# Kernel tuning notes

Measured on AMD Instinct MI355X. Metric: run time of the kernel, lower is better.

The kernel has to match this reference:

```python
import jax, jax.numpy as jnp
import numpy as np

N = 100000   # nodes
E = 300000   # edges
D_IN = 128   # input feature dim
H = 256      # hidden dim
L = 4        # GIN layers
G = 512      # graphs in batch
BN_EPS = 1e-5


def setup_inputs() -> dict:
    key = jax.random.key(0)
    ks = jax.random.split(key, 12)
    s = 0.02
    return {
        "x": jax.random.normal(ks[0], (N, D_IN), jnp.float32),
        "edge_index": jax.random.randint(ks[1], (2, E), 0, N, dtype=jnp.int32),
        "batch": jnp.sort(jax.random.randint(ks[2], (N,), 0, G, dtype=jnp.int32)),
        "W_in": jax.random.normal(ks[3], (D_IN, H), jnp.float32) * s,
        "b_in": jnp.zeros((H,), jnp.float32),
        "eps": jnp.zeros((L,), jnp.float32),           # GINConv train_eps init = 0
        "W1": jax.random.normal(ks[4], (L, H, 2 * H), jnp.float32) * s,
        "b1": jnp.zeros((L, 2 * H), jnp.float32),
        "W2": jax.random.normal(ks[5], (L, 2 * H, H), jnp.float32) * s,
        "b2": jnp.zeros((L, H), jnp.float32),
        "gamma": jnp.ones((L, H), jnp.float32),
        "beta": jnp.zeros((L, H), jnp.float32),
        "Wp1": jax.random.normal(ks[6], (H, H // 2), jnp.float32) * s,
        "bp1": jnp.zeros((H // 2,), jnp.float32),
        "Wp2": jax.random.normal(ks[7], (H // 2, 1), jnp.float32) * s,
        "bp2": jnp.zeros((1,), jnp.float32),
    }


def reference(x, edge_index, batch, W_in, b_in, eps, W1, b1, W2, b2,
              gamma, beta, Wp1, bp1, Wp2, bp2):
    src, dst = edge_index[0], edge_index[1]

    # input projection + relu
    h = jax.nn.relu(x @ W_in + b_in)  # [N, H]

    def layer(h, p):
        e, w1, bb1, w2, bb2, g, bt = p
        # GINConv: sum-aggregate neighbor messages at destination nodes
        agg = jax.ops.segment_sum(h[src], dst, num_segments=N)  # [N, H]
        z = (1.0 + e) * h + agg
        # GIN MLP: H -> 2H -> H
        z = jax.nn.relu(z @ w1 + bb1) @ w2 + bb2
        # BatchNorm over node dim (training-mode batch statistics, biased var)
        mu = jnp.mean(z, axis=0)
        var = jnp.var(z, axis=0)
        z = g * (z - mu) * jax.lax.rsqrt(var + BN_EPS) + bt
        return jax.nn.relu(z), None

    h, _ = jax.lax.scan(layer, h, (eps, W1, b1, W2, b2, gamma, beta))

    # global mean pool per graph
    sums = jax.ops.segment_sum(h, batch, num_segments=G)                       # [G, H]
    counts = jax.ops.segment_sum(jnp.ones((N, 1), h.dtype), batch, num_segments=G)
    pooled = sums / jnp.maximum(counts, 1.0)

    # predictor head (dropout is identity in eval)
    out = jax.nn.relu(pooled @ Wp1 + bp1) @ Wp2 + bp2  # [G, 1]
    return out
```

## Files before the change

kernel.cpp:

```cpp
#include <hip/hip_runtime.h>

#define NN 100000
#define NP 100096
#define EE 300000
#define DIN 128
#define HD  256
#define HD2 512
#define NL  4
#define NG  512
#define BN_EPS 1e-5f

typedef __attribute__((ext_vector_type(8))) short s8v;
typedef __attribute__((ext_vector_type(4))) float f4v;

typedef unsigned short ushort_t;

static __device__ inline ushort_t f2bf(float f) {
    unsigned u = __float_as_uint(f);
    unsigned r = (u + 0x7fffu + ((u >> 16) & 1u)) >> 16;
    return (ushort_t)r;
}
static __device__ inline float bf2f(ushort_t h) {
    return __uint_as_float(((unsigned)h) << 16);
}
static __device__ inline float blo(unsigned v) { return __uint_as_float(v << 16); }
static __device__ inline float bhi(unsigned v) { return __uint_as_float(v & 0xffff0000u); }

#define GLOAD_LDS16(g, l) __builtin_amdgcn_global_load_lds( \
    (const __attribute__((address_space(1))) unsigned int*)(const void*)(g), \
    (__attribute__((address_space(3))) unsigned int*)(void*)(l), 16, 0, 0)

#define WAITCNT_VM8 0xF78
#define WAITCNT_VM4 0xF74
#define WAITCNT_VM0 0xF70

__global__ __launch_bounds__(256) void gemm_bf16(
    const ushort_t* __restrict__ A, int lda,
    const ushort_t* __restrict__ BT, int ldb,
    const float* __restrict__ bias,
    ushort_t* __restrict__ C, int ldc,
    int K, int doRelu,
    int doStats, float* __restrict__ stats, int Mvalid)
{
    extern __shared__ char smem[];
    ushort_t* lds = (ushort_t*)smem;
    ushort_t* Cs  = lds;
    float* ssum   = (float*)(smem + 49152);
    float* ssq    = ssum + 512;

    const int tid  = threadIdx.x;
    const int w    = tid >> 6;
    const int L    = tid & 63;
    const int lm   = L & 15;
    const int q    = L >> 4;
    const int row0 = blockIdx.x * 128;
    const int col0 = blockIdx.y * 128;

    const ushort_t* gAbase = A  + (size_t)lm * lda;
    const ushort_t* gBbase = BT + (size_t)lm * ldb;

    f4v acc[2][8] = {};

    const int niter = K >> 5;

    #define STAGE(buf, k0) do {                                              \
        ushort_t* As_ = lds + (buf) * 8192;                                  \
        ushort_t* Bs_ = As_ + 4096;                                          \
        const int kk_ = (k0) + q * 8;                                        \
        _Pragma("unroll")                                                    \
        for (int i_ = 0; i_ < 2; ++i_) {                                     \
            const int tl_ = w * 2 + i_;                                      \
            GLOAD_LDS16(gAbase + (size_t)(row0 + tl_ * 16) * lda + kk_,      \
                        As_ + tl_ * 512);                                    \
            GLOAD_LDS16(gBbase + (size_t)(col0 + tl_ * 16) * ldb + kk_,      \
                        Bs_ + tl_ * 512);                                    \
        }                                                                    \
    } while (0)

    STAGE(0, 0);
    if (niter > 1) STAGE(1, 32);
    if (niter > 2) STAGE(2, 64);

    int cur = 0;
    for (int it = 0; it < niter; ++it) {
        const int rem = niter - 1 - it;
        if (rem >= 2)      __builtin_amdgcn_s_waitcnt(WAITCNT_VM8);
        else if (rem == 1) __builtin_amdgcn_s_waitcnt(WAITCNT_VM4);
        else               __builtin_amdgcn_s_waitcnt(WAITCNT_VM0);
        __builtin_amdgcn_s_barrier();

        const ushort_t* Ab = lds + cur * 8192;
        const ushort_t* Bb = Ab + 4096;
        s8v a0 = *(const s8v*)&Ab[(2 * w)     * 512 + L * 8];
        s8v a1 = *(const s8v*)&Ab[(2 * w + 1) * 512 + L * 8];
#pragma unroll
        for (int nt = 0; nt < 8; ++nt) {
            s8v b = *(const s8v*)&Bb[nt * 512 + L * 8];
            acc[0][nt] = __builtin_amdgcn_mfma_f32_16x16x32_bf16(a0, b, acc[0][nt], 0, 0, 0);
            acc[1][nt] = __builtin_amdgcn_mfma_f32_16x16x32_bf16(a1, b, acc[1][nt], 0, 0, 0);
        }
        __builtin_amdgcn_s_barrier();
        if (it + 3 < niter) STAGE(cur, (it + 3) * 32);
        cur = (cur == 2) ? 0 : cur + 1;
    }
    #undef STAGE

    __syncthreads();

    float cs[8] = {};
    float cq[8] = {};
#pragma unroll
    for (int mt = 0; mt < 2; ++mt) {
#pragma unroll
        for (int nt = 0; nt < 8; ++nt) {
            const float bj = bias[col0 + nt * 16 + lm];
            f4v v = acc[mt][nt];
#pragma unroll
            for (int r = 0; r < 4; ++r) {
                float f = v[r] + bj;
                if (doRelu) f = fmaxf(f, 0.f);
                const int row = (2 * w + mt) * 16 + q * 4 + r;
                const int col = nt * 16 + lm;
                Cs[row * 128 + col] = f2bf(f);
                if (doStats && (row0 + row) < Mvalid) {
                    cs[nt] += f;
                    cq[nt] += f * f;
                }
            }
        }
    }
    if (doStats) {
#pragma unroll
        for (int nt = 0; nt < 8; ++nt) {
            float s = cs[nt], sq = cq[nt];
            s  += __shfl_xor(s, 16, 64);  s  += __shfl_xor(s, 32, 64);
            sq += __shfl_xor(sq, 16, 64); sq += __shfl_xor(sq, 32, 64);
            cs[nt] = s; cq[nt] = sq;
        }
    }
    __syncthreads();
    if (doStats && q == 0) {
#pragma unroll
        for (int nt = 0; nt < 8; ++nt) {
            ssum[w * 128 + nt * 16 + lm] = cs[nt];
            ssq [w * 128 + nt * 16 + lm] = cq[nt];
        }
    }
#pragma unroll
    for (int i = 0; i < 8; ++i) {
        const int idx = i * 256 + tid;
        const int row = idx >> 4, ch = idx & 15;
        s8v val = *(const s8v*)&Cs[row * 128 + ch * 8];
        *(s8v*)(C + (size_t)(row0 + row) * ldc + col0 + ch * 8) = val;
    }
    if (doStats) {
        __syncthreads();
        if (tid < 128) {
            const float s  = ssum[tid] + ssum[128 + tid] + ssum[256 + tid] + ssum[384 + tid];
            const float sq = ssq[tid]  + ssq[128 + tid]  + ssq[256 + tid]  + ssq[384 + tid];
            unsafeAtomicAdd(&stats[col0 + tid], s);
            unsafeAtomicAdd(&stats[HD + col0 + tid], sq);
        }
    }
}

__global__ __launch_bounds__(256) void pack_w1_kernel(
    const float* __restrict__ W1, ushort_t* __restrict__ W1P)
{
    const int t = threadIdx.x, L = t & 63;
    const int gu = blockIdx.x * 4 + (t >> 6);
    const int l = gu >> 8, rem = gu & 255;
    const int c = rem >> 4, u = rem & 15;
    const int kk = u >> 1, nt = u & 1;
    const int h  = c * 32 + nt * 16 + (L & 15);
    const int k0 = kk * 32 + (L >> 4) * 8;
    const float* src = W1 + (size_t)l * HD * HD2;
    s8v v;
#pragma unroll
    for (int e = 0; e < 8; ++e)
        v[e] = (short)f2bf(src[(size_t)(k0 + e) * HD2 + h]);
    *(s8v*)(W1P + (size_t)gu * 512 + L * 8) = v;
}

__global__ __launch_bounds__(256) void pack_w2_kernel(
    const float* __restrict__ W2, ushort_t* __restrict__ W2P)
{
    const int t = threadIdx.x, L = t & 63;
    const int gu = blockIdx.x * 4 + (t >> 6);
    const int l = gu >> 8, rem = gu & 255;
    const int c = rem >> 4, nt = rem & 15;
    const int h  = nt * 16 + (L & 15);
    const int k0 = c * 32 + (L >> 4) * 8;
    const float* src = W2 + (size_t)l * HD2 * HD;
    s8v v;
#pragma unroll
    for (int e = 0; e < 8; ++e)
        v[e] = (short)f2bf(src[(size_t)(k0 + e) * HD + h]);
    *(s8v*)(W2P + (size_t)gu * 512 + L * 8) = v;
}

__global__ __launch_bounds__(512, 4) void fused_mlp_kernel(
    const ushort_t* __restrict__ A,
    const ushort_t* __restrict__ W1l,
    const float*    __restrict__ b1l,
    const ushort_t* __restrict__ W2l,
    const float*    __restrict__ b2l,
    ushort_t* __restrict__ C,
    float* __restrict__ stats)
{
    extern __shared__ char smem[];
    ushort_t* lds = (ushort_t*)smem;
    const int tid = threadIdx.x;
    const int w   = tid >> 6;
    const int L   = tid & 63;
    const int lm  = L & 15;
    const int q   = L >> 4;
    const int row0 = blockIdx.x * 128;

    float* b1s = (float*)(smem + 75776);
    char*  hcb = smem + 65536 + w * 1280;

    if (tid < HD2) b1s[tid] = b1l[tid];
    __syncthreads();

    const ushort_t* Arow = A + (size_t)(row0 + w * 16 + lm) * HD;
    s8v a[8];
#pragma unroll
    for (int kk = 0; kk < 8; ++kk)
        a[kk] = *(const s8v*)(Arow + kk * 32 + q * 8);
    __builtin_amdgcn_s_waitcnt(WAITCNT_VM0);

#define STAGE_W(buf, cc) do {                                                 \
    ushort_t* Wb_ = lds + (buf) * 16384;                                      \
    if (w < 4) {                                                              \
        _Pragma("unroll")                                                     \
        for (int i_ = 0; i_ < 4; ++i_) {                                      \
            const int u_ = w * 4 + i_;                                        \
            GLOAD_LDS16(W1l + ((cc) * 16 + u_) * 512 + L * 8,                 \
                        Wb_ + u_ * 512);                                      \
        }                                                                     \
    } else {                                                                  \
        _Pragma("unroll")                                                     \
        for (int i_ = 0; i_ < 4; ++i_) {                                      \
            const int u_ = (w - 4) * 4 + i_;                                  \
            GLOAD_LDS16(W2l + ((cc) * 16 + u_) * 512 + L * 8,                 \
                        Wb_ + 8192 + u_ * 512);                               \
        }                                                                     \
    }                                                                         \
} while (0)

    STAGE_W(0, 0);
    STAGE_W(1, 1);

    f4v acc2[16] = {};
    for (int c = 0; c < 16; ++c) {
        if (c < 15) __builtin_amdgcn_s_waitcnt(WAITCNT_VM4);
        else        __builtin_amdgcn_s_waitcnt(WAITCNT_VM0);
        __builtin_amdgcn_s_barrier();
        __builtin_amdgcn_sched_barrier(0);

        const ushort_t* Wb  = lds + (c & 1) * 16384;
        const ushort_t* W2b = Wb + 8192;

        f4v acc1[2] = {};
        __builtin_amdgcn_s_setprio(1);
#pragma unroll
        for (int kk = 0; kk < 8; ++kk) {
#pragma unroll
            for (int nt = 0; nt < 2; ++nt) {
                s8v b = *(const s8v*)&Wb[(kk * 2 + nt) * 512 + L * 8];
                acc1[nt] = __builtin_amdgcn_mfma_f32_16x16x32_bf16(a[kk], b, acc1[nt], 0, 0, 0);
            }
        }
        __builtin_amdgcn_s_setprio(0);

#pragma unroll
        for (int nt = 0; nt < 2; ++nt) {
            const float bj = b1s[c * 32 + nt * 16 + lm];
#pragma unroll
            for (int r = 0; r < 4; ++r) {
                const int rr = q * 4 + r;
                *(ushort_t*)(hcb + rr * 80 + (nt * 16 + lm) * 2) =
                    f2bf(fmaxf(acc1[nt][r] + bj, 0.f));
            }
        }
        const s8v at = *(const s8v*)(hcb + lm * 80 + q * 16);
        __builtin_amdgcn_s_setprio(1);
#pragma unroll
        for (int nt = 0; nt < 16; ++nt) {
            s8v b = *(const s8v*)&W2b[nt * 512 + L * 8];
            acc2[nt] = __builtin_amdgcn_mfma_f32_16x16x32_bf16(at, b, acc2[nt], 0, 0, 0);
        }
        __builtin_amdgcn_s_setprio(0);

        __builtin_amdgcn_sched_barrier(0);
        __builtin_amdgcn_s_barrier();
        if (c + 2 < 16) STAGE_W((c & 1), c + 2);
    }
#undef STAGE_W

    __syncthreads();

    ushort_t* Cs = lds;
    float* ssum  = (float*)(smem + 65536);
    float* ssq   = (float*)(smem + 73728);

#pragma unroll
    for (int nt = 0; nt < 16; ++nt) {
        const float bj = b2l[nt * 16 + lm];
        float s = 0.f, sq = 0.f;
#pragma unroll
        for (int r = 0; r < 4; ++r) {
            const float f  = acc2[nt][r] + bj;
            const int row  = w * 16 + q * 4 + r;
            Cs[row * 256 + nt * 16 + lm] = f2bf(f);
            if (row0 + row < NN) { s += f; sq += f * f; }
        }
        s  += __shfl_xor(s, 16, 64);  s  += __shfl_xor(s, 32, 64);
        sq += __shfl_xor(sq, 16, 64); sq += __shfl_xor(sq, 32, 64);
        if (q == 0) {
            ssum[w * 256 + nt * 16 + lm] = s;
            ssq [w * 256 + nt * 16 + lm] = sq;
        }
    }
    __syncthreads();

#pragma unroll
    for (int i = 0; i < 8; ++i) {
        const int idx = i * 512 + tid;
        const int row = idx >> 5, ch = idx & 31;
        const s8v v = *(const s8v*)&Cs[idx * 8];
        *(s8v*)(C + (size_t)(row0 + row) * HD + ch * 8) = v;
    }
    if (tid < HD) {
        float s = 0.f, sq = 0.f;
#pragma unroll
        for (int ww = 0; ww < 8; ++ww) {
            s  += ssum[ww * 256 + tid];
            sq += ssq [ww * 256 + tid];
        }
        unsafeAtomicAdd(&stats[tid], s);
        unsafeAtomicAdd(&stats[HD + tid], sq);
    }
}

__global__ __launch_bounds__(256) void transpose_cvt_kernel(
    const float* __restrict__ in, ushort_t* __restrict__ out, int R, int C,
    long inStride, long outStride)
{
    __shared__ float tile[32][33];
    const float* inp  = in  + (size_t)blockIdx.z * inStride;
    ushort_t*    outp = out + (size_t)blockIdx.z * outStride;
    const int bx = blockIdx.x * 32;
    const int by = blockIdx.y * 32;
    const int tx = threadIdx.x & 31;
    const int ty = threadIdx.x >> 5;
#pragma unroll
    for (int i = 0; i < 32; i += 8)
        tile[ty + i][tx] = inp[(size_t)(by + ty + i) * C + bx + tx];
    __syncthreads();
#pragma unroll
    for (int i = 0; i < 32; i += 8)
        outp[(size_t)(bx + ty + i) * R + by + tx] = f2bf(tile[tx][ty + i]);
}

__global__ __launch_bounds__(256) void cvt_kernel(
    const float* __restrict__ in, ushort_t* __restrict__ out, long n4)
{
    const long i = (long)blockIdx.x * 256 + threadIdx.x;
    if (i >= n4) return;
    const float4 v = ((const float4*)in)[i];
    ushort4 o;
    o.x = f2bf(v.x); o.y = f2bf(v.y); o.z = f2bf(v.z); o.w = f2bf(v.w);
    ((ushort4*)out)[i] = o;
}

__global__ __launch_bounds__(256) void zero_kernel(float* __restrict__ p, long n4)
{
    const long i = (long)blockIdx.x * 256 + threadIdx.x;
    if (i < n4) ((float4*)p)[i] = make_float4(0.f, 0.f, 0.f, 0.f);
}

__global__ __launch_bounds__(256) void init_bn_kernel(
    float* __restrict__ sscale, float* __restrict__ sshift,
    float* __restrict__ stats)
{
    const int t = threadIdx.x;
    sscale[t] = 1.f;
    sshift[t] = 0.f;
    stats[t] = 0.f;
    stats[HD + t] = 0.f;
}

__global__ __launch_bounds__(256) void bnprep_kernel(
    float* __restrict__ stats, const float* __restrict__ gamma,
    const float* __restrict__ beta, float* __restrict__ sscale,
    float* __restrict__ sshift, int Nn)
{
    const int t = threadIdx.x;
    const float invN = 1.0f / (float)Nn;
    const float mu  = stats[t] * invN;
    const float var = stats[HD + t] * invN - mu * mu;
    const float inv = rsqrtf(var + BN_EPS);
    const float sc  = gamma[t] * inv;
    sscale[t] = sc;
    sshift[t] = beta[t] - mu * sc;
    stats[t] = 0.f;
    stats[HD + t] = 0.f;
}

__global__ __launch_bounds__(256) void hist_kernel(
    const int* __restrict__ dst, int* __restrict__ deg, int E)
{
    const int e = blockIdx.x * 256 + threadIdx.x;
    if (e < E) atomicAdd(&deg[dst[e]], 1);
}

__global__ __launch_bounds__(256) void scan1_kernel(
    const int* __restrict__ deg, int* __restrict__ partial,
    int* __restrict__ bsums, int n)
{
    __shared__ int tmp[256];
    const int i = blockIdx.x * 256 + threadIdx.x;
    const int v = (i < n) ? deg[i] : 0;
    tmp[threadIdx.x] = v;
    __syncthreads();
    for (int off = 1; off < 256; off <<= 1) {
        const int t = (threadIdx.x >= off) ? tmp[threadIdx.x - off] : 0;
        __syncthreads();
        tmp[threadIdx.x] += t;
        __syncthreads();
    }
    if (i < n) partial[i] = tmp[threadIdx.x] - v;
    if (threadIdx.x == 255) bsums[blockIdx.x] = tmp[255];
}

__global__ __launch_bounds__(512) void scan2_kernel(int* __restrict__ bsums, int nb)
{
    __shared__ int tmp[512];
    const int i = threadIdx.x;
    const int v = (i < nb) ? bsums[i] : 0;
    tmp[i] = v;
    __syncthreads();
    for (int off = 1; off < 512; off <<= 1) {
        const int t = (i >= off) ? tmp[i - off] : 0;
        __syncthreads();
        tmp[i] += t;
        __syncthreads();
    }
    if (i < nb) bsums[i] = tmp[i] - v;
}

__global__ __launch_bounds__(256) void scan3_kernel(
    const int* __restrict__ partial, const int* __restrict__ bsums,
    int* __restrict__ offs, int* __restrict__ cursor, int n)
{
    const int i = blockIdx.x * 256 + threadIdx.x;
    if (i < n) {
        const int o = partial[i] + bsums[blockIdx.x];
        offs[i] = o;
        cursor[i] = o;
    }
}

__global__ __launch_bounds__(256) void scatter_kernel(
    const int* __restrict__ src, const int* __restrict__ dst,
    int* __restrict__ cursor, int* __restrict__ srcSorted, int E)
{
    const int e = blockIdx.x * 256 + threadIdx.x;
    if (e >= E) return;
    const int p = atomicAdd(&cursor[dst[e]], 1);
    srcSorted[p] = src[e];
}

__global__ __launch_bounds__(256) void aggregate_kernel(
    const ushort_t* __restrict__ z, const int* __restrict__ offs,
    const int* __restrict__ deg, const int* __restrict__ srcSorted,
    const float* __restrict__ epsArr, int epsIdx,
    const float* __restrict__ sscale, const float* __restrict__ sshift,
    ushort_t* __restrict__ out)
{
    const int n = blockIdx.x * 8 + (threadIdx.x >> 5);
    const int L = threadIdx.x & 31;
    const int c0 = L * 8;
    const float4 scA = *(const float4*)(sscale + c0);
    const float4 scB = *(const float4*)(sscale + c0 + 4);
    const float4 shA = *(const float4*)(sshift + c0);
    const float4 shB = *(const float4*)(sshift + c0 + 4);
    const int start = offs[n];
    const int dc = deg[n];
    float a[8] = {};
    float b[8] = {};
    int j = 0;
    for (; j + 1 < dc; j += 2) {
        const int s0 = srcSorted[start + j];
        const int s1 = srcSorted[start + j + 1];
        const uint4 u = *(const uint4*)(z + (size_t)s0 * HD + c0);
        const uint4 v = *(const uint4*)(z + (size_t)s1 * HD + c0);
        a[0] += fmaxf(blo(u.x) * scA.x + shA.x, 0.f);
        a[1] += fmaxf(bhi(u.x) * scA.y + shA.y, 0.f);
        a[2] += fmaxf(blo(u.y) * scA.z + shA.z, 0.f);
        a[3] += fmaxf(bhi(u.y) * scA.w + shA.w, 0.f);
        a[4] += fmaxf(blo(u.z) * scB.x + shB.x, 0.f);
        a[5] += fmaxf(bhi(u.z) * scB.y + shB.y, 0.f);
        a[6] += fmaxf(blo(u.w) * scB.z + shB.z, 0.f);
        a[7] += fmaxf(bhi(u.w) * scB.w + shB.w, 0.f);
        b[0] += fmaxf(blo(v.x) * scA.x + shA.x, 0.f);
        b[1] += fmaxf(bhi(v.x) * scA.y + shA.y, 0.f);
        b[2] += fmaxf(blo(v.y) * scA.z + shA.z, 0.f);
        b[3] += fmaxf(bhi(v.y) * scA.w + shA.w, 0.f);
        b[4] += fmaxf(blo(v.z) * scB.x + shB.x, 0.f);
        b[5] += fmaxf(bhi(v.z) * scB.y + shB.y, 0.f);
        b[6] += fmaxf(blo(v.w) * scB.z + shB.z, 0.f);
        b[7] += fmaxf(bhi(v.w) * scB.w + shB.w, 0.f);
    }
    if (j < dc) {
        const int s0 = srcSorted[start + j];
        const uint4 u = *(const uint4*)(z + (size_t)s0 * HD + c0);
        a[0] += fmaxf(blo(u.x) * scA.x + shA.x, 0.f);
        a[1] += fmaxf(bhi(u.x) * scA.y + shA.y, 0.f);
        a[2] += fmaxf(blo(u.y) * scA.z + shA.z, 0.f);
        a[3] += fmaxf(bhi(u.y) * scA.w + shA.w, 0.f);
        a[4] += fmaxf(blo(u.z) * scB.x + shB.x, 0.f);
        a[5] += fmaxf(bhi(u.z) * scB.y + shB.y, 0.f);
        a[6] += fmaxf(blo(u.w) * scB.z + shB.z, 0.f);
        a[7] += fmaxf(bhi(u.w) * scB.w + shB.w, 0.f);
    }
#pragma unroll
    for (int k = 0; k < 8; ++k) a[k] += b[k];
    const float se = 1.0f + epsArr[epsIdx];
    const uint4 hs = *(const uint4*)(z + (size_t)n * HD + c0);
    float y[8];
    y[0] = se * fmaxf(blo(hs.x) * scA.x + shA.x, 0.f) + a[0];
    y[1] = se * fmaxf(bhi(hs.x) * scA.y + shA.y, 0.f) + a[1];
    y[2] = se * fmaxf(blo(hs.y) * scA.z + shA.z, 0.f) + a[2];
    y[3] = se * fmaxf(bhi(hs.y) * scA.w + shA.w, 0.f) + a[3];
    y[4] = se * fmaxf(blo(hs.z) * scB.x + shB.x, 0.f) + a[4];
    y[5] = se * fmaxf(bhi(hs.z) * scB.y + shB.y, 0.f) + a[5];
    y[6] = se * fmaxf(blo(hs.w) * scB.z + shB.z, 0.f) + a[6];
    y[7] = se * fmaxf(bhi(hs.w) * scB.w + shB.w, 0.f) + a[7];
    uint4 o;
    o.x = (unsigned)f2bf(y[0]) | ((unsigned)f2bf(y[1]) << 16);
    o.y = (unsigned)f2bf(y[2]) | ((unsigned)f2bf(y[3]) << 16);
    o.z = (unsigned)f2bf(y[4]) | ((unsigned)f2bf(y[5]) << 16);
    o.w = (unsigned)f2bf(y[6]) | ((unsigned)f2bf(y[7]) << 16);
    *(uint4*)(out + (size_t)n * HD + c0) = o;
}

__global__ __launch_bounds__(256) void pool_head_kernel(
    const ushort_t* __restrict__ z, const int* __restrict__ batch,
    const float* __restrict__ sscale, const float* __restrict__ sshift,
    const float* __restrict__ Wp1, const float* __restrict__ bp1,
    const float* __restrict__ Wp2, const float* __restrict__ bp2,
    float* __restrict__ out)
{
    __shared__ float poolw[4][HD];
    __shared__ float pool[HD];
    __shared__ float red[128];
    __shared__ int seg[2];
    const int g = blockIdx.x;
    const int t = threadIdx.x;
    const int w = t >> 6;
    const int L = t & 63;
    if (t == 0) {
        int lo = 0, hi = NN;
        while (lo < hi) { const int m = (lo + hi) >> 1; if (batch[m] < g) lo = m + 1; else hi = m; }
        seg[0] = lo;
        hi = NN;
        while (lo < hi) { const int m = (lo + hi) >> 1; if (batch[m] < g + 1) lo = m + 1; else hi = m; }
        seg[1] = lo;
    }
    __syncthreads();
    const int start = seg[0], end = seg[1];
    const int c0 = L * 4;
    const float4 sc = *(const float4*)(sscale + c0);
    const float4 sh = *(const float4*)(sshift + c0);
    float a0 = 0.f, a1 = 0.f, a2 = 0.f, a3 = 0.f;
    float b0 = 0.f, b1 = 0.f, b2 = 0.f, b3 = 0.f;
    int r = start + w;
    for (; r + 4 < end; r += 8) {
        const ushort4 u = *(const ushort4*)(z + (size_t)r * HD + c0);
        const ushort4 v = *(const ushort4*)(z + (size_t)(r + 4) * HD + c0);
        a0 += fmaxf(bf2f(u.x) * sc.x + sh.x, 0.f);
        a1 += fmaxf(bf2f(u.y) * sc.y + sh.y, 0.f);
        a2 += fmaxf(bf2f(u.z) * sc.z + sh.z, 0.f);
        a3 += fmaxf(bf2f(u.w) * sc.w + sh.w, 0.f);
        b0 += fmaxf(bf2f(v.x) * sc.x + sh.x, 0.f);
        b1 += fmaxf(bf2f(v.y) * sc.y + sh.y, 0.f);
        b2 += fmaxf(bf2f(v.z) * sc.z + sh.z, 0.f);
        b3 += fmaxf(bf2f(v.w) * sc.w + sh.w, 0.f);
    }
    if (r < end) {
        const ushort4 u = *(const ushort4*)(z + (size_t)r * HD + c0);
        a0 += fmaxf(bf2f(u.x) * sc.x + sh.x, 0.f);
        a1 += fmaxf(bf2f(u.y) * sc.y + sh.y, 0.f);
        a2 += fmaxf(bf2f(u.z) * sc.z + sh.z, 0.f);
        a3 += fmaxf(bf2f(u.w) * sc.w + sh.w, 0.f);
    }
    poolw[w][c0 + 0] = a0 + b0;
    poolw[w][c0 + 1] = a1 + b1;
    poolw[w][c0 + 2] = a2 + b2;
    poolw[w][c0 + 3] = a3 + b3;
    __syncthreads();
    const float invC = 1.0f / (float)max(end - start, 1);
    pool[t] = (poolw[0][t] + poolw[1][t] + poolw[2][t] + poolw[3][t]) * invC;
    __syncthreads();
    if (t < 128) {
        float acc = 0.f;
#pragma unroll 4
        for (int k = 0; k < HD; ++k)
            acc += pool[k] * Wp1[k * 128 + t];
        red[t] = fmaxf(acc + bp1[t], 0.f) * Wp2[t];
    }
    __syncthreads();
    for (int sft = 64; sft > 0; sft >>= 1) {
        if (t < sft) red[t] += red[t + sft];
        __syncthreads();
    }
    if (t == 0) out[g] = red[0] + bp2[0];
}

extern "C" void kernel_launch(void* const* d_in, const int* in_sizes, int n_in,
                              void* d_out, int out_size, void* d_ws, size_t ws_size,
                              hipStream_t stream)
{
    const float* x     = (const float*)d_in[0];
    const int*   ei    = (const int*)  d_in[1];
    const int*   batch = (const int*)  d_in[2];
    const float* W_in  = (const float*)d_in[3];
    const float* b_in  = (const float*)d_in[4];
    const float* eps   = (const float*)d_in[5];
    const float* W1    = (const float*)d_in[6];
    const float* b1    = (const float*)d_in[7];
    const float* W2    = (const float*)d_in[8];
    const float* b2    = (const float*)d_in[9];
    const float* gamma = (const float*)d_in[10];
    const float* beta  = (const float*)d_in[11];
    const float* Wp1   = (const float*)d_in[12];
    const float* bp1   = (const float*)d_in[13];
    const float* Wp2   = (const float*)d_in[14];
    const float* bp2   = (const float*)d_in[15];

    const int* srcIdx = ei;
    const int* dstIdx = ei + EE;

    char* p = (char*)d_ws;
    ushort_t* zbuf    = (ushort_t*)p;  p += (size_t)NP * HD  * 2;
    ushort_t* abuf    = (ushort_t*)p;  p += (size_t)NP * HD  * 2;
    ushort_t* hidden  = (ushort_t*)p;  p += (size_t)NP * HD2 * 2;
    ushort_t* W1P     = (ushort_t*)p;  p += (size_t)NL * HD2 * HD * 2;
    ushort_t* W2P     = (ushort_t*)p;  p += (size_t)NL * HD * HD2 * 2;
    ushort_t* WinT    = (ushort_t*)p;  p += (size_t)HD * DIN * 2;
    int* deg          = (int*)p;       p += (size_t)NN * 4;
    int* partial      = (int*)p;       p += (size_t)NN * 4;
    int* bsums        = (int*)p;       p += 512 * 4;
    int* offs         = (int*)p;       p += (size_t)NN * 4;
    int* cursor       = (int*)p;       p += (size_t)NN * 4;
    int* srcSorted    = (int*)p;       p += (size_t)EE * 4;
    float* stats      = (float*)p;     p += 2 * HD * 4;
    float* sscale     = (float*)p;     p += HD * 4;
    float* sshift     = (float*)p;     p += HD * 4;
    ushort_t* x_bf    = hidden;

    const int nb = (NN + 255) / 256;
    const int GEMM_LDS  = 53248;
    const int FUSED_LDS = 81920;

    init_bn_kernel<<<1, 256, 0, stream>>>(sscale, sshift, stats);

    transpose_cvt_kernel<<<dim3(HD / 32, DIN / 32, 1), 256, 0, stream>>>(
        W_in, WinT, DIN, HD, 0, 0);
    pack_w1_kernel<<<256, 256, 0, stream>>>(W1, W1P);
    pack_w2_kernel<<<256, 256, 0, stream>>>(W2, W2P);
    cvt_kernel<<<(int)(((long)NN * DIN / 4 + 255) / 256), 256, 0, stream>>>(
        x, x_bf, (long)NN * DIN / 4);

    zero_kernel<<<(NN / 4 + 255) / 256, 256, 0, stream>>>((float*)deg, NN / 4);
    hist_kernel<<<(EE + 255) / 256, 256, 0, stream>>>(dstIdx, deg, EE);
    scan1_kernel<<<nb, 256, 0, stream>>>(deg, partial, bsums, NN);
    scan2_kernel<<<1, 512, 0, stream>>>(bsums, nb);
    scan3_kernel<<<nb, 256, 0, stream>>>(partial, bsums, offs, cursor, NN);
    scatter_kernel<<<(EE + 255) / 256, 256, 0, stream>>>(srcIdx, dstIdx, cursor, srcSorted, EE);

    gemm_bf16<<<dim3(NP / 128, HD / 128), 256, GEMM_LDS, stream>>>(
        x_bf, DIN, WinT, DIN, b_in, zbuf, HD, DIN, 1, 0, nullptr, 0);

    for (int l = 0; l < NL; ++l) {
        aggregate_kernel<<<NN / 8, 256, 0, stream>>>(
            zbuf, offs, deg, srcSorted, eps, l, sscale, sshift, abuf);

        fused_mlp_kernel<<<NP / 128, 512, FUSED_LDS, stream>>>(
            abuf, W1P + (size_t)l * HD2 * HD, b1 + (size_t)l * HD2,
            W2P + (size_t)l * HD * HD2, b2 + (size_t)l * HD, zbuf, stats);

        bnprep_kernel<<<1, 256, 0, stream>>>(
            stats, gamma + (size_t)l * HD, beta + (size_t)l * HD, sscale, sshift, NN);
    }

    pool_head_kernel<<<NG, 256, 0, stream>>>(zbuf, batch, sscale, sshift,
                                             Wp1, bp1, Wp2, bp2, (float*)d_out);
}
```

Measured before the change: 735.5 us.

## Give each wave two M-tiles in fused MLP, halving block threads

The fused MLP kernel now runs 256 threads (4 waves) per 128-row block instead of 8 waves, and each wave handles 32 rows as two 16-row MFMA tiles. Each weight fragment read from LDS now feeds two MFMAs, which halves LDS weight traffic per FLOP. Staging loads and the stats reduction are reworked to match. The cost is doubled accumulator registers (32 f4v for acc2), which may limit occupancy or cause spills, and fewer waves to hide latency.

```diff
diff --git a/kernel.cpp b/kernel.cpp
--- a/kernel.cpp
+++ b/kernel.cpp
@@ -199,7 +199,7 @@
     *(s8v*)(W2P + (size_t)gu * 512 + L * 8) = v;
 }
 
-__global__ __launch_bounds__(512, 4) void fused_mlp_kernel(
+__global__ __launch_bounds__(256, 2) void fused_mlp_kernel(
     const ushort_t* __restrict__ A,
     const ushort_t* __restrict__ W1l,
     const float*    __restrict__ b1l,
@@ -218,31 +218,35 @@
     const int row0 = blockIdx.x * 128;
 
     float* b1s = (float*)(smem + 75776);
-    char*  hcb = smem + 65536 + w * 1280;
-
-    if (tid < HD2) b1s[tid] = b1l[tid];
-    __syncthreads();
-
-    const ushort_t* Arow = A + (size_t)(row0 + w * 16 + lm) * HD;
-    s8v a[8];
-#pragma unroll
-    for (int kk = 0; kk < 8; ++kk)
-        a[kk] = *(const s8v*)(Arow + kk * 32 + q * 8);
+    char*  hcb = smem + 65536 + w * 2560;
+
+    b1s[tid]       = b1l[tid];
+    b1s[256 + tid] = b1l[256 + tid];
+    __syncthreads();
+
+    s8v a[2][8];
+#pragma unroll
+    for (int mt = 0; mt < 2; ++mt) {
+        const ushort_t* Arow = A + (size_t)(row0 + w * 32 + mt * 16 + lm) * HD;
+#pragma unroll
+        for (int kk = 0; kk < 8; ++kk)
+            a[mt][kk] = *(const s8v*)(Arow + kk * 32 + q * 8);
+    }
     __builtin_amdgcn_s_waitcnt(WAITCNT_VM0);
 
 #define STAGE_W(buf, cc) do {                                                 \
     ushort_t* Wb_ = lds + (buf) * 16384;                                      \
-    if (w < 4) {                                                              \
+    if (w < 2) {                                                              \
         _Pragma("unroll")                                                     \
-        for (int i_ = 0; i_ < 4; ++i_) {                                      \
-            const int u_ = w * 4 + i_;                                        \
+        for (int i_ = 0; i_ < 8; ++i_) {                                      \
+            const int u_ = w * 8 + i_;                                        \
             GLOAD_LDS16(W1l + ((cc) * 16 + u_) * 512 + L * 8,                 \
                         Wb_ + u_ * 512);                                      \
         }                                                                     \
     } else {                                                                  \
         _Pragma("unroll")                                                     \
-        for (int i_ = 0; i_ < 4; ++i_) {                                      \
-            const int u_ = (w - 4) * 4 + i_;                                  \
+        for (int i_ = 0; i_ < 8; ++i_) {                                      \
+            const int u_ = (w - 2) * 8 + i_;                                  \
             GLOAD_LDS16(W2l + ((cc) * 16 + u_) * 512 + L * 8,                 \
                         Wb_ + 8192 + u_ * 512);                               \
         }                                                                     \
@@ -252,9 +256,9 @@
     STAGE_W(0, 0);
     STAGE_W(1, 1);
 
-    f4v acc2[16] = {};
+    f4v acc2[2][16] = {};
     for (int c = 0; c < 16; ++c) {
-        if (c < 15) __builtin_amdgcn_s_waitcnt(WAITCNT_VM4);
+        if (c < 15) __builtin_amdgcn_s_waitcnt(WAITCNT_VM8);
         else        __builtin_amdgcn_s_waitcnt(WAITCNT_VM0);
         __builtin_amdgcn_s_barrier();
         __builtin_amdgcn_sched_barrier(0);
@@ -262,34 +266,40 @@
         const ushort_t* Wb  = lds + (c & 1) * 16384;
         const ushort_t* W2b = Wb + 8192;
 
-        f4v acc1[2] = {};
+        f4v acc1[2][2] = {};
         __builtin_amdgcn_s_setprio(1);
 #pragma unroll
         for (int kk = 0; kk < 8; ++kk) {
 #pragma unroll
             for (int nt = 0; nt < 2; ++nt) {
                 s8v b = *(const s8v*)&Wb[(kk * 2 + nt) * 512 + L * 8];
-                acc1[nt] = __builtin_amdgcn_mfma_f32_16x16x32_bf16(a[kk], b, acc1[nt], 0, 0, 0);
+                acc1[0][nt] = __builtin_amdgcn_mfma_f32_16x16x32_bf16(a[0][kk], b, acc1[0][nt], 0, 0, 0);
+                acc1[1][nt] = __builtin_amdgcn_mfma_f32_16x16x32_bf16(a[1][kk], b, acc1[1][nt], 0, 0, 0);
             }
         }
         __builtin_amdgcn_s_setprio(0);
 
 #pragma unroll
-        for (int nt = 0; nt < 2; ++nt) {
-            const float bj = b1s[c * 32 + nt * 16 + lm];
-#pragma unroll
-            for (int r = 0; r < 4; ++r) {
-                const int rr = q * 4 + r;
-                *(ushort_t*)(hcb + rr * 80 + (nt * 16 + lm) * 2) =
-                    f2bf(fmaxf(acc1[nt][r] + bj, 0.f));
+        for (int mt = 0; mt < 2; ++mt) {
+#pragma unroll
+            for (int nt = 0; nt < 2; ++nt) {
+                const float bj = b1s[c * 32 + nt * 16 + lm];
+#pragma unroll
+                for (int r = 0; r < 4; ++r) {
+                    const int rr = mt * 16 + q * 4 + r;
+                    *(ushort_t*)(hcb + rr * 80 + (nt * 16 + lm) * 2) =
+                        f2bf(fmaxf(acc1[mt][nt][r] + bj, 0.f));
+                }
             }
         }
-        const s8v at = *(const s8v*)(hcb + lm * 80 + q * 16);
+        s8v at0 = *(const s8v*)(hcb + lm * 80 + q * 16);
+        s8v at1 = *(const s8v*)(hcb + (16 + lm) * 80 + q * 16);
         __builtin_amdgcn_s_setprio(1);
 #pragma unroll
         for (int nt = 0; nt < 16; ++nt) {
             s8v b = *(const s8v*)&W2b[nt * 512 + L * 8];
-            acc2[nt] = __builtin_amdgcn_mfma_f32_16x16x32_bf16(at, b, acc2[nt], 0, 0, 0);
+            acc2[0][nt] = __builtin_amdgcn_mfma_f32_16x16x32_bf16(at0, b, acc2[0][nt], 0, 0, 0);
+            acc2[1][nt] = __builtin_amdgcn_mfma_f32_16x16x32_bf16(at1, b, acc2[1][nt], 0, 0, 0);
         }
         __builtin_amdgcn_s_setprio(0);
 
@@ -303,18 +313,21 @@
 
     ushort_t* Cs = lds;
     float* ssum  = (float*)(smem + 65536);
-    float* ssq   = (float*)(smem + 73728);
+    float* ssq   = (float*)(smem + 69632);
 
 #pragma unroll
     for (int nt = 0; nt < 16; ++nt) {
         const float bj = b2l[nt * 16 + lm];
         float s = 0.f, sq = 0.f;
 #pragma unroll
-        for (int r = 0; r < 4; ++r) {
-            const float f  = acc2[nt][r] + bj;
-            const int row  = w * 16 + q * 4 + r;
-            Cs[row * 256 + nt * 16 + lm] = f2bf(f);
-            if (row0 + row < NN) { s += f; sq += f * f; }
+        for (int mt = 0; mt < 2; ++mt) {
+#pragma unroll
+            for (int r = 0; r < 4; ++r) {
+                const float f  = acc2[mt][nt][r] + bj;
+                const int row  = w * 32 + mt * 16 + q * 4 + r;
+                Cs[row * 256 + nt * 16 + lm] = f2bf(f);
+                if (row0 + row < NN) { s += f; sq += f * f; }
+            }
         }
         s  += __shfl_xor(s, 16, 64);  s  += __shfl_xor(s, 32, 64);
         sq += __shfl_xor(sq, 16, 64); sq += __shfl_xor(sq, 32, 64);
@@ -326,19 +339,15 @@
     __syncthreads();
 
 #pragma unroll
-    for (int i = 0; i < 8; ++i) {
-        const int idx = i * 512 + tid;
+    for (int i = 0; i < 16; ++i) {
+        const int idx = i * 256 + tid;
         const int row = idx >> 5, ch = idx & 31;
         const s8v v = *(const s8v*)&Cs[idx * 8];
         *(s8v*)(C + (size_t)(row0 + row) * HD + ch * 8) = v;
     }
-    if (tid < HD) {
-        float s = 0.f, sq = 0.f;
-#pragma unroll
-        for (int ww = 0; ww < 8; ++ww) {
-            s  += ssum[ww * 256 + tid];
-            sq += ssq [ww * 256 + tid];
-        }
+    {
+        const float s  = ssum[tid] + ssum[256 + tid] + ssum[512 + tid] + ssum[768 + tid];
+        const float sq = ssq[tid]  + ssq[256 + tid]  + ssq[512 + tid]  + ssq[768 + tid];
         unsafeAtomicAdd(&stats[tid], s);
         unsafeAtomicAdd(&stats[HD + tid], sq);
     }
@@ -664,7 +673,7 @@
 
     const int nb = (NN + 255) / 256;
     const int GEMM_LDS  = 53248;
-    const int FUSED_LDS = 81920;
+    const int FUSED_LDS = 77824;
 
     init_bn_kernel<<<1, 256, 0, stream>>>(sscale, sshift, stats);
 
@@ -689,7 +698,7 @@
         aggregate_kernel<<<NN / 8, 256, 0, stream>>>(
             zbuf, offs, deg, srcSorted, eps, l, sscale, sshift, abuf);
 
-        fused_mlp_kernel<<<NP / 128, 512, FUSED_LDS, stream>>>(
+        fused_mlp_kernel<<<NP / 128, 256, FUSED_LDS, stream>>>(
             abuf, W1P + (size_t)l * HD2 * HD, b1 + (size_t)l * HD2,
             W2P + (size_t)l * HD * HD2, b2 + (size_t)l * HD, zbuf, stats);
 
```

Result: no change. 734.2 us (-0.2%).

## Software-pipeline fused MLP so second GEMM lags first by one chunk

Applied to the files above, without the earlier changes.

Restructures the fused H->2H->H MLP loop so the W2 GEMM for chunk i-1 runs in the same iteration as the W1 GEMM for chunk i. W1 and W2 staging buffers are split into separate double buffers with W2 staged one step behind. The aim is to hide the LDS round-trip of the ReLU intermediate (write then read hcb) behind independent MFMA work. In exchange it adds a peeled epilogue iteration and extra control flow. The b1 bias load now runs for every thread without the tid guard, which is only correct if the block has at most 512 threads.

```diff
diff --git a/kernel.cpp b/kernel.cpp
--- a/kernel.cpp
+++ b/kernel.cpp
@@ -220,7 +220,7 @@
     float* b1s = (float*)(smem + 75776);
     char*  hcb = smem + 65536 + w * 1280;
 
-    if (tid < HD2) b1s[tid] = b1l[tid];
+    b1s[tid] = b1l[tid];
     __syncthreads();
 
     const ushort_t* Arow = A + (size_t)(row0 + w * 16 + lm) * HD;
@@ -230,37 +230,45 @@
         a[kk] = *(const s8v*)(Arow + kk * 32 + q * 8);
     __builtin_amdgcn_s_waitcnt(WAITCNT_VM0);
 
-#define STAGE_W(buf, cc) do {                                                 \
-    ushort_t* Wb_ = lds + (buf) * 16384;                                      \
+#define STAGE_W1(buf, cc) do {                                                \
     if (w < 4) {                                                              \
+        ushort_t* Wb_ = lds + (buf) * 8192;                                   \
         _Pragma("unroll")                                                     \
         for (int i_ = 0; i_ < 4; ++i_) {                                      \
             const int u_ = w * 4 + i_;                                        \
             GLOAD_LDS16(W1l + ((cc) * 16 + u_) * 512 + L * 8,                 \
                         Wb_ + u_ * 512);                                      \
         }                                                                     \
-    } else {                                                                  \
+    }                                                                         \
+} while (0)
+#define STAGE_W2(buf, cc) do {                                                \
+    if (w >= 4) {                                                             \
+        ushort_t* Wb_ = lds + 16384 + (buf) * 8192;                           \
         _Pragma("unroll")                                                     \
         for (int i_ = 0; i_ < 4; ++i_) {                                      \
             const int u_ = (w - 4) * 4 + i_;                                  \
             GLOAD_LDS16(W2l + ((cc) * 16 + u_) * 512 + L * 8,                 \
-                        Wb_ + 8192 + u_ * 512);                               \
+                        Wb_ + u_ * 512);                                      \
         }                                                                     \
     }                                                                         \
 } while (0)
 
-    STAGE_W(0, 0);
-    STAGE_W(1, 1);
+    STAGE_W1(0, 0);
+    STAGE_W2(0, 0);
+    STAGE_W1(1, 1);
 
     f4v acc2[16] = {};
-    for (int c = 0; c < 16; ++c) {
-        if (c < 15) __builtin_amdgcn_s_waitcnt(WAITCNT_VM4);
+    for (int i = 0; i < 16; ++i) {
+        if (i < 15) __builtin_amdgcn_s_waitcnt(WAITCNT_VM4);
         else        __builtin_amdgcn_s_waitcnt(WAITCNT_VM0);
         __builtin_amdgcn_s_barrier();
         __builtin_amdgcn_sched_barrier(0);
 
-        const ushort_t* Wb  = lds + (c & 1) * 16384;
-        const ushort_t* W2b = Wb + 8192;
+        s8v at = {};
+        if (i > 0) at = *(const s8v*)(hcb + lm * 80 + q * 16);
+
+        const ushort_t* Wb  = lds + (i & 1) * 8192;
+        const ushort_t* W2b = lds + 16384 + ((i - 1) & 1) * 8192;
 
         f4v acc1[2] = {};
         __builtin_amdgcn_s_setprio(1);
@@ -276,7 +284,7 @@
 
 #pragma unroll
         for (int nt = 0; nt < 2; ++nt) {
-            const float bj = b1s[c * 32 + nt * 16 + lm];
+            const float bj = b1s[i * 32 + nt * 16 + lm];
 #pragma unroll
             for (int r = 0; r < 4; ++r) {
                 const int rr = q * 4 + r;
@@ -284,6 +292,27 @@
                     f2bf(fmaxf(acc1[nt][r] + bj, 0.f));
             }
         }
+
+        if (i > 0) {
+            __builtin_amdgcn_s_setprio(1);
+#pragma unroll
+            for (int nt = 0; nt < 16; ++nt) {
+                s8v b = *(const s8v*)&W2b[nt * 512 + L * 8];
+                acc2[nt] = __builtin_amdgcn_mfma_f32_16x16x32_bf16(at, b, acc2[nt], 0, 0, 0);
+            }
+            __builtin_amdgcn_s_setprio(0);
+        }
+
+        __builtin_amdgcn_sched_barrier(0);
+        __builtin_amdgcn_s_barrier();
+        if (i <= 13) STAGE_W1(i & 1, i + 2);
+        if (i <= 14) STAGE_W2((i + 1) & 1, i + 1);
+    }
+#undef STAGE_W1
+#undef STAGE_W2
+
+    {
+        const ushort_t* W2b = lds + 16384 + (15 & 1) * 8192;
         const s8v at = *(const s8v*)(hcb + lm * 80 + q * 16);
         __builtin_amdgcn_s_setprio(1);
 #pragma unroll
@@ -292,12 +321,7 @@
             acc2[nt] = __builtin_amdgcn_mfma_f32_16x16x32_bf16(at, b, acc2[nt], 0, 0, 0);
         }
         __builtin_amdgcn_s_setprio(0);
-
-        __builtin_amdgcn_sched_barrier(0);
-        __builtin_amdgcn_s_barrier();
-        if (c + 2 < 16) STAGE_W((c & 1), c + 2);
-    }
-#undef STAGE_W
+    }
 
     __syncthreads();
 
```

Result: slower. 767.2 us (+4.3%).

## Fuse neighbor aggregation into the fused MLP kernel with ping-pong buffers

Applied to the files above, without the earlier changes.

Removes the separate aggregate kernel and performs the GIN sum-aggregation (BN-apply, ReLU, eps self term) directly while loading the A fragments in the fused MLP kernel. Output now goes to an alternate buffer, since the kernel reads z from arbitrary neighbor rows, and the buffers swap every layer. This saves a full write and re-read of the aggregated activation plus one launch per layer. The cost is that the gather now runs inside a heavy, occupancy-limited MFMA kernel with one lane per row and a serial edge loop, so load latency is poorly hidden and work is imbalanced across degrees.

```diff
diff --git a/kernel.cpp b/kernel.cpp
--- a/kernel.cpp
+++ b/kernel.cpp
@@ -25,6 +25,19 @@
 }
 static __device__ inline float blo(unsigned v) { return __uint_as_float(v << 16); }
 static __device__ inline float bhi(unsigned v) { return __uint_as_float(v & 0xffff0000u); }
+
+static __device__ inline void gacc(float* A, const uint4 u,
+                                   const float4 s0, const float4 s1,
+                                   const float4 h0, const float4 h1, float wg) {
+    A[0] += wg * fmaxf(blo(u.x) * s0.x + h0.x, 0.f);
+    A[1] += wg * fmaxf(bhi(u.x) * s0.y + h0.y, 0.f);
+    A[2] += wg * fmaxf(blo(u.y) * s0.z + h0.z, 0.f);
+    A[3] += wg * fmaxf(bhi(u.y) * s0.w + h0.w, 0.f);
+    A[4] += wg * fmaxf(blo(u.z) * s1.x + h1.x, 0.f);
+    A[5] += wg * fmaxf(bhi(u.z) * s1.y + h1.y, 0.f);
+    A[6] += wg * fmaxf(blo(u.w) * s1.z + h1.z, 0.f);
+    A[7] += wg * fmaxf(bhi(u.w) * s1.w + h1.w, 0.f);
+}
 
 #define GLOAD_LDS16(g, l) __builtin_amdgcn_global_load_lds( \
     (const __attribute__((address_space(1))) unsigned int*)(const void*)(g), \
@@ -199,8 +212,12 @@
     *(s8v*)(W2P + (size_t)gu * 512 + L * 8) = v;
 }
 
-__global__ __launch_bounds__(512, 4) void fused_mlp_kernel(
-    const ushort_t* __restrict__ A,
+__global__ __launch_bounds__(512, 4) void fused_layer_kernel(
+    const ushort_t* __restrict__ z,
+    const int* __restrict__ offs, const int* __restrict__ deg,
+    const int* __restrict__ srcSorted,
+    const float* __restrict__ epsArr, int epsIdx,
+    const float* __restrict__ sscale, const float* __restrict__ sshift,
     const ushort_t* __restrict__ W1l,
     const float*    __restrict__ b1l,
     const ushort_t* __restrict__ W2l,
@@ -220,14 +237,50 @@
     float* b1s = (float*)(smem + 75776);
     char*  hcb = smem + 65536 + w * 1280;
 
-    if (tid < HD2) b1s[tid] = b1l[tid];
-    __syncthreads();
-
-    const ushort_t* Arow = A + (size_t)(row0 + w * 16 + lm) * HD;
+    b1s[tid] = b1l[tid];
+    __syncthreads();
+
+    const int n = row0 + w * 16 + lm;
+    int estart = 0, edeg = 0;
+    if (n < NN) { estart = offs[n]; edeg = deg[n]; }
+    const float se = 1.0f + epsArr[epsIdx];
     s8v a[8];
 #pragma unroll
-    for (int kk = 0; kk < 8; ++kk)
-        a[kk] = *(const s8v*)(Arow + kk * 32 + q * 8);
+    for (int p = 0; p < 4; ++p) {
+        const int c0 = (2 * p) * 32 + q * 8;
+        const int c1 = c0 + 32;
+        const float4 sa0 = *(const float4*)(sscale + c0);
+        const float4 sa1 = *(const float4*)(sscale + c0 + 4);
+        const float4 ha0 = *(const float4*)(sshift + c0);
+        const float4 ha1 = *(const float4*)(sshift + c0 + 4);
+        const float4 sb0 = *(const float4*)(sscale + c1);
+        const float4 sb1 = *(const float4*)(sscale + c1 + 4);
+        const float4 hb0 = *(const float4*)(sshift + c1);
+        const float4 hb1 = *(const float4*)(sshift + c1 + 4);
+        float A0[8] = {};
+        float A1[8] = {};
+        if (n < NN) {
+            const uint4 u = *(const uint4*)(z + (size_t)n * HD + c0);
+            const uint4 v = *(const uint4*)(z + (size_t)n * HD + c1);
+            gacc(A0, u, sa0, sa1, ha0, ha1, se);
+            gacc(A1, v, sb0, sb1, hb0, hb1, se);
+        }
+        for (int j = 0; j < edeg; ++j) {
+            const int s = srcSorted[estart + j];
+            const uint4 u = *(const uint4*)(z + (size_t)s * HD + c0);
+            const uint4 v = *(const uint4*)(z + (size_t)s * HD + c1);
+            gacc(A0, u, sa0, sa1, ha0, ha1, 1.f);
+            gacc(A1, v, sb0, sb1, hb0, hb1, 1.f);
+        }
+        s8v va, vb;
+#pragma unroll
+        for (int e = 0; e < 8; ++e) {
+            va[e] = (short)f2bf(A0[e]);
+            vb[e] = (short)f2bf(A1[e]);
+        }
+        a[2 * p]     = va;
+        a[2 * p + 1] = vb;
+    }
     __builtin_amdgcn_s_waitcnt(WAITCNT_VM0);
 
 #define STAGE_W(buf, cc) do {                                                 \
@@ -473,80 +526,6 @@
     srcSorted[p] = src[e];
 }
 
-__global__ __launch_bounds__(256) void aggregate_kernel(
-    const ushort_t* __restrict__ z, const int* __restrict__ offs,
-    const int* __restrict__ deg, const int* __restrict__ srcSorted,
-    const float* __restrict__ epsArr, int epsIdx,
-    const float* __restrict__ sscale, const float* __restrict__ sshift,
-    ushort_t* __restrict__ out)
-{
-    const int n = blockIdx.x * 8 + (threadIdx.x >> 5);
-    const int L = threadIdx.x & 31;
-    const int c0 = L * 8;
-    const float4 scA = *(const float4*)(sscale + c0);
-    const float4 scB = *(const float4*)(sscale + c0 + 4);
-    const float4 shA = *(const float4*)(sshift + c0);
-    const float4 shB = *(const float4*)(sshift + c0 + 4);
-    const int start = offs[n];
-    const int dc = deg[n];
-    float a[8] = {};
-    float b[8] = {};
-    int j = 0;
-    for (; j + 1 < dc; j += 2) {
-        const int s0 = srcSorted[start + j];
-        const int s1 = srcSorted[start + j + 1];
-        const uint4 u = *(const uint4*)(z + (size_t)s0 * HD + c0);
-        const uint4 v = *(const uint4*)(z + (size_t)s1 * HD + c0);
-        a[0] += fmaxf(blo(u.x) * scA.x + shA.x, 0.f);
-        a[1] += fmaxf(bhi(u.x) * scA.y + shA.y, 0.f);
-        a[2] += fmaxf(blo(u.y) * scA.z + shA.z, 0.f);
-        a[3] += fmaxf(bhi(u.y) * scA.w + shA.w, 0.f);
-        a[4] += fmaxf(blo(u.z) * scB.x + shB.x, 0.f);
-        a[5] += fmaxf(bhi(u.z) * scB.y + shB.y, 0.f);
-        a[6] += fmaxf(blo(u.w) * scB.z + shB.z, 0.f);
-        a[7] += fmaxf(bhi(u.w) * scB.w + shB.w, 0.f);
-        b[0] += fmaxf(blo(v.x) * scA.x + shA.x, 0.f);
-        b[1] += fmaxf(bhi(v.x) * scA.y + shA.y, 0.f);
-        b[2] += fmaxf(blo(v.y) * scA.z + shA.z, 0.f);
-        b[3] += fmaxf(bhi(v.y) * scA.w + shA.w, 0.f);
-        b[4] += fmaxf(blo(v.z) * scB.x + shB.x, 0.f);
-        b[5] += fmaxf(bhi(v.z) * scB.y + shB.y, 0.f);
-        b[6] += fmaxf(blo(v.w) * scB.z + shB.z, 0.f);
-        b[7] += fmaxf(bhi(v.w) * scB.w + shB.w, 0.f);
-    }
-    if (j < dc) {
-        const int s0 = srcSorted[start + j];
-        const uint4 u = *(const uint4*)(z + (size_t)s0 * HD + c0);
-        a[0] += fmaxf(blo(u.x) * scA.x + shA.x, 0.f);
-        a[1] += fmaxf(bhi(u.x) * scA.y + shA.y, 0.f);
-        a[2] += fmaxf(blo(u.y) * scA.z + shA.z, 0.f);
-        a[3] += fmaxf(bhi(u.y) * scA.w + shA.w, 0.f);
-        a[4] += fmaxf(blo(u.z) * scB.x + shB.x, 0.f);
-        a[5] += fmaxf(bhi(u.z) * scB.y + shB.y, 0.f);
-        a[6] += fmaxf(blo(u.w) * scB.z + shB.z, 0.f);
-        a[7] += fmaxf(bhi(u.w) * scB.w + shB.w, 0.f);
-    }
-#pragma unroll
-    for (int k = 0; k < 8; ++k) a[k] += b[k];
-    const float se = 1.0f + epsArr[epsIdx];
-    const uint4 hs = *(const uint4*)(z + (size_t)n * HD + c0);
-    float y[8];
-    y[0] = se * fmaxf(blo(hs.x) * scA.x + shA.x, 0.f) + a[0];
-    y[1] = se * fmaxf(bhi(hs.x) * scA.y + shA.y, 0.f) + a[1];
-    y[2] = se * fmaxf(blo(hs.y) * scA.z + shA.z, 0.f) + a[2];
-    y[3] = se * fmaxf(bhi(hs.y) * scA.w + shA.w, 0.f) + a[3];
-    y[4] = se * fmaxf(blo(hs.z) * scB.x + shB.x, 0.f) + a[4];
-    y[5] = se * fmaxf(bhi(hs.z) * scB.y + shB.y, 0.f) + a[5];
-    y[6] = se * fmaxf(blo(hs.w) * scB.z + shB.z, 0.f) + a[6];
-    y[7] = se * fmaxf(bhi(hs.w) * scB.w + shB.w, 0.f) + a[7];
-    uint4 o;
-    o.x = (unsigned)f2bf(y[0]) | ((unsigned)f2bf(y[1]) << 16);
-    o.y = (unsigned)f2bf(y[2]) | ((unsigned)f2bf(y[3]) << 16);
-    o.z = (unsigned)f2bf(y[4]) | ((unsigned)f2bf(y[5]) << 16);
-    o.w = (unsigned)f2bf(y[6]) | ((unsigned)f2bf(y[7]) << 16);
-    *(uint4*)(out + (size_t)n * HD + c0) = o;
-}
-
 __global__ __launch_bounds__(256) void pool_head_kernel(
     const ushort_t* __restrict__ z, const int* __restrict__ batch,
     const float* __restrict__ sscale, const float* __restrict__ sshift,
@@ -646,7 +625,7 @@
 
     char* p = (char*)d_ws;
     ushort_t* zbuf    = (ushort_t*)p;  p += (size_t)NP * HD  * 2;
-    ushort_t* abuf    = (ushort_t*)p;  p += (size_t)NP * HD  * 2;
+    ushort_t* zalt    = (ushort_t*)p;  p += (size_t)NP * HD  * 2;
     ushort_t* hidden  = (ushort_t*)p;  p += (size_t)NP * HD2 * 2;
     ushort_t* W1P     = (ushort_t*)p;  p += (size_t)NL * HD2 * HD * 2;
     ushort_t* W2P     = (ushort_t*)p;  p += (size_t)NL * HD * HD2 * 2;
@@ -685,18 +664,22 @@
     gemm_bf16<<<dim3(NP / 128, HD / 128), 256, GEMM_LDS, stream>>>(
         x_bf, DIN, WinT, DIN, b_in, zbuf, HD, DIN, 1, 0, nullptr, 0);
 
+    const ushort_t* zin = zbuf;
+    ushort_t*       zout = zalt;
     for (int l = 0; l < NL; ++l) {
-        aggregate_kernel<<<NN / 8, 256, 0, stream>>>(
-            zbuf, offs, deg, srcSorted, eps, l, sscale, sshift, abuf);
-
-        fused_mlp_kernel<<<NP / 128, 512, FUSED_LDS, stream>>>(
-            abuf, W1P + (size_t)l * HD2 * HD, b1 + (size_t)l * HD2,
-            W2P + (size_t)l * HD * HD2, b2 + (size_t)l * HD, zbuf, stats);
+        fused_layer_kernel<<<NP / 128, 512, FUSED_LDS, stream>>>(
+            zin, offs, deg, srcSorted, eps, l, sscale, sshift,
+            W1P + (size_t)l * HD2 * HD, b1 + (size_t)l * HD2,
+            W2P + (size_t)l * HD * HD2, b2 + (size_t)l * HD, zout, stats);
 
         bnprep_kernel<<<1, 256, 0, stream>>>(
             stats, gamma + (size_t)l * HD, beta + (size_t)l * HD, sscale, sshift, NN);
-    }
-
-    pool_head_kernel<<<NG, 256, 0, stream>>>(zbuf, batch, sscale, sshift,
+
+        const ushort_t* t = zin;
+        zin = zout;
+        zout = (ushort_t*)t;
+    }
+
+    pool_head_kernel<<<NG, 256, 0, stream>>>(zin, batch, sscale, sshift,
                                              Wp1, bp1, Wp2, bp2, (float*)d_out);
 }
```

Measured after the change: 797.9 us. 1.08x slower.
